# Kernel tuning notes

Hardware: AMD Instinct MI355X
Metric: run time of the kernel (lower is better)

Reference implementation:

```python
import jax, jax.numpy as jnp
import numpy as np

B, N, E = 8, 100000, 3200000
LAMBDA_PHYSICS = 1.0

def setup_inputs() -> dict:
    key = jax.random.key(0)
    k1, k2, k3, k4, k5 = jax.random.split(key, 5)
    node_heads = jax.random.normal(k1, (B, N), dtype=jnp.float32)
    demands = jax.random.normal(k2, (B, N), dtype=jnp.float32)
    edge_index = jax.random.randint(k3, (2, E), 0, N, dtype=jnp.int64)
    edge_attr = jax.random.uniform(k4, (E, 2), dtype=jnp.float32)
    reservoir_nodes = jax.random.randint(k5, (64,), 0, N, dtype=jnp.int64)
    reservoir_head = jnp.ones((1,), dtype=jnp.float32)
    return {"node_heads": node_heads, "demands": demands, "edge_index": edge_index,
            "edge_attr": edge_attr, "reservoir_nodes": reservoir_nodes,
            "reservoir_head": reservoir_head}

def reference(node_heads, demands, edge_index, edge_attr, reservoir_nodes, reservoir_head):
    src, dst = edge_index[0], edge_index[1]
    conductances = edge_attr[:, 0]  # [E]
    # Pipe flow: Q_e = g_e * (h_src - h_dst), shape [B, E]
    head_diff = node_heads[:, src] - node_heads[:, dst]
    flows = conductances[None, :] * head_diff
    # Continuity: vectorized scatter-add replacing the per-edge Python loop
    net_flows = jnp.zeros_like(node_heads).at[:, src].add(flows).at[:, dst].add(-flows)
    violations = net_flows - demands
    continuity_loss = jnp.mean(violations ** 2)
    # Boundary: reservoir heads pinned to reservoir_head
    pred_res = node_heads[:, reservoir_nodes]  # [B, n_res]
    boundary_loss = jnp.mean((pred_res - reservoir_head[0]) ** 2)
    total_physics_loss = (continuity_loss + boundary_loss) * LAMBDA_PHYSICS
    return continuity_loss, boundary_loss, total_physics_loss, flows
```

## Files before the change

kernel.cpp:

```cpp
#include <hip/hip_runtime.h>

#define B 8
#define N 100000
#define NE 3200000
#define CHUNK2_LOG 7
#define CHUNK2 128
#define NCHUNK2 782
#define CAP2 9216
#define CAPH 4800
#define EPB 2048
#define RPB (2 * EPB)
#define SCANW 1024

typedef float f32x4 __attribute__((ext_vector_type(4)));
typedef unsigned u32x2 __attribute__((ext_vector_type(2)));

__device__ u32x2 g_rec2[(size_t)NCHUNK2 * CAP2];
__device__ int   g_cursor2[NCHUNK2];
__device__ float g_heads_t[N * B];
__device__ float g_accum;

__global__ __launch_bounds__(256) void zero_kernel() {
    for (int i = threadIdx.x; i < NCHUNK2; i += 256) g_cursor2[i] = 0;
    if (threadIdx.x == 0) g_accum = 0.0f;
}

__global__ __launch_bounds__(256) void transpose_kernel(
    const float* __restrict__ node_heads)
{
    int i = blockIdx.x * blockDim.x + threadIdx.x;
    if (i >= N * B) return;
    int n = i >> 3, b = i & 7;
    g_heads_t[i] = node_heads[b * N + n];
}

__global__ __launch_bounds__(256) void phase1_kernel(
    const int* __restrict__ edge_index,
    const float* __restrict__ edge_attr,
    float* __restrict__ flows_out)
{
    __shared__ int   hist[NCHUNK2];
    __shared__ int   lbase[NCHUNK2];
    __shared__ int   gbase[NCHUNK2];
    __shared__ int   lcur[NCHUNK2];
    __shared__ int   scanbuf[SCANW];
    __shared__ u32x2 s_rec[RPB];

    int tid = threadIdx.x;
    int e0 = blockIdx.x * EPB;

    for (int i = tid; i < NCHUNK2; i += 256) hist[i] = 0;
    __syncthreads();

    for (int i = tid; i < EPB; i += 256) {
        int e = e0 + i;
        if (e < NE) {
            int s = edge_index[e];
            int d = edge_index[NE + e];
            atomicAdd(&hist[s >> CHUNK2_LOG], 1);
            atomicAdd(&hist[d >> CHUNK2_LOG], 1);
        }
    }
    __syncthreads();

    for (int i = tid; i < SCANW; i += 256)
        scanbuf[i] = (i < NCHUNK2) ? hist[i] : 0;
    __syncthreads();
    for (int off = 1; off < SCANW; off <<= 1) {
        int v[SCANW / 256];
#pragma unroll
        for (int j = 0; j < SCANW / 256; ++j) {
            int i = tid + j * 256;
            v[j] = (i >= off) ? scanbuf[i - off] : 0;
        }
        __syncthreads();
#pragma unroll
        for (int j = 0; j < SCANW / 256; ++j) {
            int i = tid + j * 256;
            if (i >= off) scanbuf[i] += v[j];
        }
        __syncthreads();
    }
    for (int i = tid; i < NCHUNK2; i += 256) {
        int lb = scanbuf[i] - hist[i];
        lbase[i] = lb;
        lcur[i]  = lb;
        gbase[i] = atomicAdd(&g_cursor2[i], hist[i]);
    }
    __syncthreads();

    for (int i = tid; i < EPB; i += 256) {
        int e = e0 + i;
        if (e >= NE) continue;
        int s = edge_index[e];
        int d = edge_index[NE + e];
        float c = edge_attr[2 * (size_t)e];

        const f32x4* hs4 = (const f32x4*)&g_heads_t[s << 3];
        const f32x4* hd4 = (const f32x4*)&g_heads_t[d << 3];
        f32x4 a0 = hs4[0], a1 = hs4[1];
        f32x4 b0 = hd4[0], b1 = hd4[1];
        f32x4 f0 = c * (a0 - b0);
        f32x4 f1 = c * (a1 - b1);

        __builtin_nontemporal_store(f0.x, &flows_out[0 * NE + e]);
        __builtin_nontemporal_store(f0.y, &flows_out[1 * NE + e]);
        __builtin_nontemporal_store(f0.z, &flows_out[2 * NE + e]);
        __builtin_nontemporal_store(f0.w, &flows_out[3 * NE + e]);
        __builtin_nontemporal_store(f1.x, &flows_out[4 * NE + e]);
        __builtin_nontemporal_store(f1.y, &flows_out[5 * NE + e]);
        __builtin_nontemporal_store(f1.z, &flows_out[6 * NE + e]);
        __builtin_nontemporal_store(f1.w, &flows_out[7 * NE + e]);

        unsigned cb = __float_as_uint(c);
        int ks = s >> CHUNK2_LOG;
        int sl = atomicAdd(&lcur[ks], 1);
        u32x2 rs; rs.x = ((unsigned)(s & (CHUNK2 - 1)) << 17) | (unsigned)d; rs.y = cb;
        s_rec[sl] = rs;
        int kd = d >> CHUNK2_LOG;
        sl = atomicAdd(&lcur[kd], 1);
        u32x2 rd; rd.x = ((unsigned)(d & (CHUNK2 - 1)) << 17) | (unsigned)s; rd.y = cb;
        s_rec[sl] = rd;
    }
    __syncthreads();

    int wave = tid >> 6, lane = tid & 63;
    for (int k = wave; k < NCHUNK2; k += 4) {
        int cnt = hist[k];
        if (cnt == 0) continue;
        int lb = lbase[k], gb = gbase[k];
        u32x2* dst = &g_rec2[(size_t)k * CAP2];
        for (int i = lane; i < cnt; i += 64) {
            if (gb + i < CAP2)
                __builtin_nontemporal_store(s_rec[lb + i], &dst[gb + i]);
        }
    }
}

__global__ __launch_bounds__(256) void sortgather_kernel(
    const float* __restrict__ demands)
{
    __shared__ u32x2 s_rec[CAPH];
    __shared__ int   hist[64];
    __shared__ int   hbase[64];
    __shared__ int   hcur[64];
    __shared__ int   scanbuf[64];
    __shared__ float wred[4];

    int tid = threadIdx.x;
    int c = blockIdx.x;
    int cnt = g_cursor2[c];
    if (cnt > CAP2) cnt = CAP2;
    const u32x2* rec = &g_rec2[(size_t)c * CAP2];

    float contrib = 0.0f;

    for (int h = 0; h < 2; ++h) {
        if (tid < 64) hist[tid] = 0;
        __syncthreads();

        for (int i = tid; i < cnt; i += 256) {
            int ml = (int)(rec[i].x >> 17);
            if ((ml >> 6) == h) atomicAdd(&hist[ml & 63], 1);
        }
        __syncthreads();

        if (tid < 64) scanbuf[tid] = hist[tid];
        __syncthreads();
        for (int off = 1; off < 64; off <<= 1) {
            int v = (tid < 64 && tid >= off) ? scanbuf[tid - off] : 0;
            __syncthreads();
            if (tid < 64 && tid >= off) scanbuf[tid] += v;
            __syncthreads();
        }
        if (tid < 64) {
            int b0 = scanbuf[tid] - hist[tid];
            hbase[tid] = b0;
            hcur[tid]  = b0;
        }
        __syncthreads();

        for (int i = tid; i < cnt; i += 256) {
            u32x2 r = rec[i];
            int ml = (int)(r.x >> 17);
            if ((ml >> 6) == h) {
                int sl = atomicAdd(&hcur[ml & 63], 1);
                if (sl < CAPH) {
                    u32x2 rr; rr.x = r.x & 0x1FFFFu; rr.y = r.y;
                    s_rec[sl] = rr;
                }
            }
        }
        __syncthreads();

        int nl = tid >> 2, p = tid & 3;
        int n = (c << CHUNK2_LOG) + (h << 6) + nl;
        int off0 = hbase[nl];
        int cn = hist[nl];
        if (off0 + cn > CAPH) cn = (CAPH > off0) ? (CAPH - off0) : 0;
        int nc = (n < N) ? n : 0;
        const f32x4* hm = (const f32x4*)&g_heads_t[nc << 3];
        f32x4 m0 = hm[0], m1 = hm[1];
        f32x4 a0 = {0.f, 0.f, 0.f, 0.f};
        f32x4 a1 = {0.f, 0.f, 0.f, 0.f};
        for (int i = p; i < cn; i += 4) {
            u32x2 r = s_rec[off0 + i];
            float cc = __uint_as_float(r.y);
            const f32x4* ho = (const f32x4*)&g_heads_t[r.x << 3];
            f32x4 o0 = ho[0], o1 = ho[1];
            a0 += cc * (m0 - o0);
            a1 += cc * (m1 - o1);
        }
        float acc[8] = {a0.x, a0.y, a0.z, a0.w, a1.x, a1.y, a1.z, a1.w};
        bool emit = (p == 0) && (n < N);
#pragma unroll
        for (int j = 0; j < 8; ++j) {
            float v = acc[j];
            v += __shfl_xor(v, 1, 64);
            v += __shfl_xor(v, 2, 64);
            if (emit) {
                float vv = v - demands[j * N + n];
                contrib = fmaf(vv, vv, contrib);
            }
        }
        __syncthreads();
    }

    for (int off = 32; off > 0; off >>= 1)
        contrib += __shfl_down(contrib, off, 64);
    int wave = tid >> 6, lane = tid & 63;
    if (lane == 0) wred[wave] = contrib;
    __syncthreads();
    if (tid == 0)
        unsafeAtomicAdd(&g_accum, wred[0] + wred[1] + wred[2] + wred[3]);
}

__global__ __launch_bounds__(512) void finalize_kernel(
    const float* __restrict__ node_heads,
    const int* __restrict__ res_nodes,
    const float* __restrict__ res_head,
    float* __restrict__ out)
{
    __shared__ float ssum[8];
    int t = threadIdx.x;
    int b = t >> 6;
    int j = t & 63;
    float pred = node_heads[b * N + res_nodes[j]];
    float diff = pred - res_head[0];
    float local = diff * diff;
    for (int off = 32; off > 0; off >>= 1)
        local += __shfl_down(local, off, 64);
    if ((t & 63) == 0) ssum[t >> 6] = local;
    __syncthreads();
    if (t == 0) {
        float bsum = 0.0f;
        for (int w = 0; w < 8; ++w) bsum += ssum[w];
        float boundary = bsum / 512.0f;
        float continuity = g_accum / (float)(B * N);
        out[0] = continuity;
        out[1] = boundary;
        out[2] = continuity + boundary;
    }
}

extern "C" void kernel_launch(void* const* d_in, const int* in_sizes, int n_in,
                              void* d_out, int out_size, void* d_ws, size_t ws_size,
                              hipStream_t stream) {
    const float* node_heads = (const float*)d_in[0];
    const float* demands    = (const float*)d_in[1];
    const int*   edge_index = (const int*)d_in[2];
    const float* edge_attr  = (const float*)d_in[3];
    const int*   res_nodes  = (const int*)d_in[4];
    const float* res_head   = (const float*)d_in[5];

    float* out = (float*)d_out;

    zero_kernel<<<1, 256, 0, stream>>>();
    transpose_kernel<<<(N * B + 255) / 256, 256, 0, stream>>>(node_heads);
    phase1_kernel<<<(NE + EPB - 1) / EPB, 256, 0, stream>>>(
        edge_index, edge_attr, out + 3);
    sortgather_kernel<<<NCHUNK2, 256, 0, stream>>>(demands);
    finalize_kernel<<<1, 512, 0, stream>>>(node_heads, res_nodes, res_head, out);
}
```

Baseline: 501.7 us.

## Replace shared-memory atomics with wave-ballot match aggregation in both bucketing kernels

```diff
diff --git a/kernel.cpp b/kernel.cpp
--- a/kernel.cpp
+++ b/kernel.cpp
@@ -7,9 +7,9 @@
 #define CHUNK2 128
 #define NCHUNK2 782
 #define CAP2 9216
-#define CAPH 4800
 #define EPB 2048
 #define RPB (2 * EPB)
+#define NWIN (EPB / 64)
 #define SCANW 1024
 
 typedef float f32x4 __attribute__((ext_vector_type(4)));
@@ -39,32 +39,56 @@
     const float* __restrict__ edge_attr,
     float* __restrict__ flows_out)
 {
-    __shared__ int   hist[NCHUNK2];
-    __shared__ int   lbase[NCHUNK2];
+    __shared__ u32x2 s_rec[RPB];
+    __shared__ int   wh[4 * NCHUNK2];
+    __shared__ int   lbase[NCHUNK2 + 1];
     __shared__ int   gbase[NCHUNK2];
-    __shared__ int   lcur[NCHUNK2];
-    __shared__ int   scanbuf[SCANW];
-    __shared__ u32x2 s_rec[RPB];
-
-    int tid = threadIdx.x;
+
+    int tid  = threadIdx.x;
+    int wave = tid >> 6, lane = tid & 63;
+    unsigned long long lanebit = 1ull << lane;
     int e0 = blockIdx.x * EPB;
 
-    for (int i = tid; i < NCHUNK2; i += 256) hist[i] = 0;
-    __syncthreads();
-
-    for (int i = tid; i < EPB; i += 256) {
-        int e = e0 + i;
-        if (e < NE) {
-            int s = edge_index[e];
-            int d = edge_index[NE + e];
-            atomicAdd(&hist[s >> CHUNK2_LOG], 1);
-            atomicAdd(&hist[d >> CHUNK2_LOG], 1);
-        }
-    }
-    __syncthreads();
-
-    for (int i = tid; i < SCANW; i += 256)
-        scanbuf[i] = (i < NCHUNK2) ? hist[i] : 0;
+    for (int i = tid; i < 4 * NCHUNK2; i += 256) wh[i] = 0;
+    __syncthreads();
+
+    for (int t = wave; t < NWIN; t += 4) {
+        int idx = t * 64 + lane;
+        int e = e0 + idx;
+        bool v = e < NE;
+        int s = 0, d = 0;
+        if (v) { s = edge_index[e]; d = edge_index[NE + e]; }
+        unsigned long long vm = __ballot(v);
+
+        unsigned ks = (unsigned)s >> CHUNK2_LOG;
+        unsigned long long m = vm;
+#pragma unroll
+        for (int b = 0; b < 10; ++b) {
+            unsigned long long bal = __ballot((ks >> b) & 1);
+            m &= ((ks >> b) & 1) ? bal : ~bal;
+        }
+        int ldr = m ? (__ffsll(m) - 1) : 0;
+        if (v && lane == ldr) wh[wave * NCHUNK2 + ks] += __popcll(m);
+
+        unsigned kd = (unsigned)d >> CHUNK2_LOG;
+        unsigned long long m2 = vm;
+#pragma unroll
+        for (int b = 0; b < 10; ++b) {
+            unsigned long long bal = __ballot((kd >> b) & 1);
+            m2 &= ((kd >> b) & 1) ? bal : ~bal;
+        }
+        int ldr2 = m2 ? (__ffsll(m2) - 1) : 0;
+        if (v && lane == ldr2) wh[wave * NCHUNK2 + kd] += __popcll(m2);
+    }
+    __syncthreads();
+
+    int* scanbuf = (int*)s_rec;
+    for (int i = tid; i < SCANW; i += 256) {
+        int tot = 0;
+        if (i < NCHUNK2)
+            tot = wh[i] + wh[NCHUNK2 + i] + wh[2 * NCHUNK2 + i] + wh[3 * NCHUNK2 + i];
+        scanbuf[i] = tot;
+    }
     __syncthreads();
     for (int off = 1; off < SCANW; off <<= 1) {
         int v[SCANW / 256];
@@ -81,54 +105,97 @@
         }
         __syncthreads();
     }
-    for (int i = tid; i < NCHUNK2; i += 256) {
-        int lb = scanbuf[i] - hist[i];
-        lbase[i] = lb;
-        lcur[i]  = lb;
-        gbase[i] = atomicAdd(&g_cursor2[i], hist[i]);
-    }
-    __syncthreads();
-
-    for (int i = tid; i < EPB; i += 256) {
-        int e = e0 + i;
-        if (e >= NE) continue;
-        int s = edge_index[e];
-        int d = edge_index[NE + e];
-        float c = edge_attr[2 * (size_t)e];
-
-        const f32x4* hs4 = (const f32x4*)&g_heads_t[s << 3];
-        const f32x4* hd4 = (const f32x4*)&g_heads_t[d << 3];
-        f32x4 a0 = hs4[0], a1 = hs4[1];
-        f32x4 b0 = hd4[0], b1 = hd4[1];
-        f32x4 f0 = c * (a0 - b0);
-        f32x4 f1 = c * (a1 - b1);
-
-        __builtin_nontemporal_store(f0.x, &flows_out[0 * NE + e]);
-        __builtin_nontemporal_store(f0.y, &flows_out[1 * NE + e]);
-        __builtin_nontemporal_store(f0.z, &flows_out[2 * NE + e]);
-        __builtin_nontemporal_store(f0.w, &flows_out[3 * NE + e]);
-        __builtin_nontemporal_store(f1.x, &flows_out[4 * NE + e]);
-        __builtin_nontemporal_store(f1.y, &flows_out[5 * NE + e]);
-        __builtin_nontemporal_store(f1.z, &flows_out[6 * NE + e]);
-        __builtin_nontemporal_store(f1.w, &flows_out[7 * NE + e]);
-
-        unsigned cb = __float_as_uint(c);
-        int ks = s >> CHUNK2_LOG;
-        int sl = atomicAdd(&lcur[ks], 1);
-        u32x2 rs; rs.x = ((unsigned)(s & (CHUNK2 - 1)) << 17) | (unsigned)d; rs.y = cb;
-        s_rec[sl] = rs;
-        int kd = d >> CHUNK2_LOG;
-        sl = atomicAdd(&lcur[kd], 1);
-        u32x2 rd; rd.x = ((unsigned)(d & (CHUNK2 - 1)) << 17) | (unsigned)s; rd.y = cb;
-        s_rec[sl] = rd;
-    }
-    __syncthreads();
-
-    int wave = tid >> 6, lane = tid & 63;
+    for (int k = tid; k < NCHUNK2; k += 256) {
+        int c0 = wh[k], c1 = wh[NCHUNK2 + k], c2 = wh[2 * NCHUNK2 + k], c3 = wh[3 * NCHUNK2 + k];
+        int tot = c0 + c1 + c2 + c3;
+        int incl = scanbuf[k];
+        int lb = incl - tot;
+        lbase[k] = lb;
+        if (k == NCHUNK2 - 1) lbase[NCHUNK2] = incl;
+        wh[k] = lb;
+        wh[NCHUNK2 + k] = lb + c0;
+        wh[2 * NCHUNK2 + k] = lb + c0 + c1;
+        wh[3 * NCHUNK2 + k] = lb + c0 + c1 + c2;
+        gbase[k] = atomicAdd(&g_cursor2[k], tot);
+    }
+    __syncthreads();
+
+    for (int t = wave; t < NWIN; t += 4) {
+        int idx = t * 64 + lane;
+        int e = e0 + idx;
+        bool v = e < NE;
+        int s = 0, d = 0; float cond = 0.0f;
+        if (v) {
+            s = edge_index[e];
+            d = edge_index[NE + e];
+            cond = edge_attr[2 * (size_t)e];
+        }
+        if (v) {
+            const f32x4* hs4 = (const f32x4*)&g_heads_t[s << 3];
+            const f32x4* hd4 = (const f32x4*)&g_heads_t[d << 3];
+            f32x4 a0 = hs4[0], a1 = hs4[1];
+            f32x4 b0 = hd4[0], b1 = hd4[1];
+            f32x4 f0 = cond * (a0 - b0);
+            f32x4 f1 = cond * (a1 - b1);
+            __builtin_nontemporal_store(f0.x, &flows_out[0 * NE + e]);
+            __builtin_nontemporal_store(f0.y, &flows_out[1 * NE + e]);
+            __builtin_nontemporal_store(f0.z, &flows_out[2 * NE + e]);
+            __builtin_nontemporal_store(f0.w, &flows_out[3 * NE + e]);
+            __builtin_nontemporal_store(f1.x, &flows_out[4 * NE + e]);
+            __builtin_nontemporal_store(f1.y, &flows_out[5 * NE + e]);
+            __builtin_nontemporal_store(f1.z, &flows_out[6 * NE + e]);
+            __builtin_nontemporal_store(f1.w, &flows_out[7 * NE + e]);
+        }
+        unsigned cb = __float_as_uint(cond);
+        unsigned long long vm = __ballot(v);
+
+        unsigned ks = (unsigned)s >> CHUNK2_LOG;
+        unsigned long long m = vm;
+#pragma unroll
+        for (int b = 0; b < 10; ++b) {
+            unsigned long long bal = __ballot((ks >> b) & 1);
+            m &= ((ks >> b) & 1) ? bal : ~bal;
+        }
+        int ldr = m ? (__ffsll(m) - 1) : 0;
+        int old = 0;
+        if (v && lane == ldr) {
+            int* p = &wh[wave * NCHUNK2 + ks];
+            old = *p; *p = old + __popcll(m);
+        }
+        old = __shfl(old, ldr, 64);
+        if (v) {
+            int slot = old + __popcll(m & (lanebit - 1));
+            u32x2 rr; rr.x = ((unsigned)(s & (CHUNK2 - 1)) << 17) | (unsigned)d; rr.y = cb;
+            s_rec[slot] = rr;
+        }
+
+        unsigned kd = (unsigned)d >> CHUNK2_LOG;
+        unsigned long long m2 = vm;
+#pragma unroll
+        for (int b = 0; b < 10; ++b) {
+            unsigned long long bal = __ballot((kd >> b) & 1);
+            m2 &= ((kd >> b) & 1) ? bal : ~bal;
+        }
+        int ldr2 = m2 ? (__ffsll(m2) - 1) : 0;
+        int old2 = 0;
+        if (v && lane == ldr2) {
+            int* p = &wh[wave * NCHUNK2 + kd];
+            old2 = *p; *p = old2 + __popcll(m2);
+        }
+        old2 = __shfl(old2, ldr2, 64);
+        if (v) {
+            int slot = old2 + __popcll(m2 & (lanebit - 1));
+            u32x2 rr; rr.x = ((unsigned)(d & (CHUNK2 - 1)) << 17) | (unsigned)s; rr.y = cb;
+            s_rec[slot] = rr;
+        }
+    }
+    __syncthreads();
+
     for (int k = wave; k < NCHUNK2; k += 4) {
-        int cnt = hist[k];
+        int lb = lbase[k];
+        int cnt = lbase[k + 1] - lb;
         if (cnt == 0) continue;
-        int lb = lbase[k], gb = gbase[k];
+        int gb = gbase[k];
         u32x2* dst = &g_rec2[(size_t)k * CAP2];
         for (int i = lane; i < cnt; i += 64) {
             if (gb + i < CAP2)
@@ -140,76 +207,124 @@
 __global__ __launch_bounds__(256) void sortgather_kernel(
     const float* __restrict__ demands)
 {
-    __shared__ u32x2 s_rec[CAPH];
-    __shared__ int   hist[64];
-    __shared__ int   hbase[64];
-    __shared__ int   hcur[64];
-    __shared__ int   scanbuf[64];
+    __shared__ u32x2 s_rec[CAP2];
+    __shared__ int   wh[4 * CHUNK2];
+    __shared__ int   hist[CHUNK2];
+    __shared__ int   hbase[CHUNK2];
+    __shared__ int   scanbuf[CHUNK2];
     __shared__ float wred[4];
 
-    int tid = threadIdx.x;
+    int tid  = threadIdx.x;
+    int wave = tid >> 6, lane = tid & 63;
+    unsigned long long lanebit = 1ull << lane;
     int c = blockIdx.x;
     int cnt = g_cursor2[c];
     if (cnt > CAP2) cnt = CAP2;
     const u32x2* rec = &g_rec2[(size_t)c * CAP2];
+    int nwin = (cnt + 63) >> 6;
+
+    for (int i = tid; i < 4 * CHUNK2; i += 256) wh[i] = 0;
+    __syncthreads();
+
+    for (int t = wave; t < nwin; t += 4) {
+        int i = t * 64 + lane;
+        bool v = i < cnt;
+        unsigned key = 0;
+        if (v) key = rec[i].x >> 17;
+        unsigned long long m = __ballot(v);
+#pragma unroll
+        for (int b = 0; b < 7; ++b) {
+            unsigned long long bal = __ballot((key >> b) & 1);
+            m &= ((key >> b) & 1) ? bal : ~bal;
+        }
+        int ldr = m ? (__ffsll(m) - 1) : 0;
+        if (v && lane == ldr) wh[wave * CHUNK2 + key] += __popcll(m);
+    }
+    __syncthreads();
+
+    if (tid < CHUNK2) {
+        int c0 = wh[tid], c1 = wh[CHUNK2 + tid], c2 = wh[2 * CHUNK2 + tid], c3 = wh[3 * CHUNK2 + tid];
+        int tot = c0 + c1 + c2 + c3;
+        hist[tid] = tot;
+        scanbuf[tid] = tot;
+    }
+    __syncthreads();
+    for (int off = 1; off < CHUNK2; off <<= 1) {
+        int vv = (tid < CHUNK2 && tid >= off) ? scanbuf[tid - off] : 0;
+        __syncthreads();
+        if (tid < CHUNK2 && tid >= off) scanbuf[tid] += vv;
+        __syncthreads();
+    }
+    if (tid < CHUNK2) {
+        int lb = scanbuf[tid] - hist[tid];
+        hbase[tid] = lb;
+        int c0 = wh[tid], c1 = wh[CHUNK2 + tid], c2 = wh[2 * CHUNK2 + tid];
+        wh[tid] = lb;
+        wh[CHUNK2 + tid] = lb + c0;
+        wh[2 * CHUNK2 + tid] = lb + c0 + c1;
+        wh[3 * CHUNK2 + tid] = lb + c0 + c1 + c2;
+    }
+    __syncthreads();
+
+    for (int t = wave; t < nwin; t += 4) {
+        int i = t * 64 + lane;
+        bool v = i < cnt;
+        u32x2 r; r.x = 0; r.y = 0;
+        if (v) r = rec[i];
+        unsigned key = r.x >> 17;
+        unsigned long long m = __ballot(v);
+#pragma unroll
+        for (int b = 0; b < 7; ++b) {
+            unsigned long long bal = __ballot((key >> b) & 1);
+            m &= ((key >> b) & 1) ? bal : ~bal;
+        }
+        int ldr = m ? (__ffsll(m) - 1) : 0;
+        int old = 0;
+        if (v && lane == ldr) {
+            int* p = &wh[wave * CHUNK2 + key];
+            old = *p; *p = old + __popcll(m);
+        }
+        old = __shfl(old, ldr, 64);
+        if (v) {
+            int slot = old + __popcll(m & (lanebit - 1));
+            s_rec[slot] = r;
+        }
+    }
+    __syncthreads();
 
     float contrib = 0.0f;
-
-    for (int h = 0; h < 2; ++h) {
-        if (tid < 64) hist[tid] = 0;
-        __syncthreads();
-
-        for (int i = tid; i < cnt; i += 256) {
-            int ml = (int)(rec[i].x >> 17);
-            if ((ml >> 6) == h) atomicAdd(&hist[ml & 63], 1);
-        }
-        __syncthreads();
-
-        if (tid < 64) scanbuf[tid] = hist[tid];
-        __syncthreads();
-        for (int off = 1; off < 64; off <<= 1) {
-            int v = (tid < 64 && tid >= off) ? scanbuf[tid - off] : 0;
-            __syncthreads();
-            if (tid < 64 && tid >= off) scanbuf[tid] += v;
-            __syncthreads();
-        }
-        if (tid < 64) {
-            int b0 = scanbuf[tid] - hist[tid];
-            hbase[tid] = b0;
-            hcur[tid]  = b0;
-        }
-        __syncthreads();
-
-        for (int i = tid; i < cnt; i += 256) {
-            u32x2 r = rec[i];
-            int ml = (int)(r.x >> 17);
-            if ((ml >> 6) == h) {
-                int sl = atomicAdd(&hcur[ml & 63], 1);
-                if (sl < CAPH) {
-                    u32x2 rr; rr.x = r.x & 0x1FFFFu; rr.y = r.y;
-                    s_rec[sl] = rr;
-                }
-            }
-        }
-        __syncthreads();
-
-        int nl = tid >> 2, p = tid & 3;
-        int n = (c << CHUNK2_LOG) + (h << 6) + nl;
+    {
+        int nl = tid >> 1, p = tid & 1;
+        int n = (c << CHUNK2_LOG) + nl;
         int off0 = hbase[nl];
         int cn = hist[nl];
-        if (off0 + cn > CAPH) cn = (CAPH > off0) ? (CAPH - off0) : 0;
         int nc = (n < N) ? n : 0;
         const f32x4* hm = (const f32x4*)&g_heads_t[nc << 3];
         f32x4 m0 = hm[0], m1 = hm[1];
         f32x4 a0 = {0.f, 0.f, 0.f, 0.f};
         f32x4 a1 = {0.f, 0.f, 0.f, 0.f};
-        for (int i = p; i < cn; i += 4) {
-            u32x2 r = s_rec[off0 + i];
-            float cc = __uint_as_float(r.y);
-            const f32x4* ho = (const f32x4*)&g_heads_t[r.x << 3];
-            f32x4 o0 = ho[0], o1 = ho[1];
-            a0 += cc * (m0 - o0);
-            a1 += cc * (m1 - o1);
+        int i = p;
+        for (; i + 2 < cn; i += 4) {
+            u32x2 r0 = s_rec[off0 + i];
+            u32x2 r1 = s_rec[off0 + i + 2];
+            float c0 = __uint_as_float(r0.y);
+            float c1 = __uint_as_float(r1.y);
+            const f32x4* ho0 = (const f32x4*)&g_heads_t[(r0.x & 0x1FFFFu) << 3];
+            const f32x4* ho1 = (const f32x4*)&g_heads_t[(r1.x & 0x1FFFFu) << 3];
+            f32x4 o00 = ho0[0], o01 = ho0[1];
+            f32x4 o10 = ho1[0], o11 = ho1[1];
+            a0 += c0 * (m0 - o00);
+            a1 += c0 * (m1 - o01);
+            a0 += c1 * (m0 - o10);
+            a1 += c1 * (m1 - o11);
+        }
+        for (; i < cn; i += 2) {
+            u32x2 r0 = s_rec[off0 + i];
+            float c0 = __uint_as_float(r0.y);
+            const f32x4* ho0 = (const f32x4*)&g_heads_t[(r0.x & 0x1FFFFu) << 3];
+            f32x4 o00 = ho0[0], o01 = ho0[1];
+            a0 += c0 * (m0 - o00);
+            a1 += c0 * (m1 - o01);
         }
         float acc[8] = {a0.x, a0.y, a0.z, a0.w, a1.x, a1.y, a1.z, a1.w};
         bool emit = (p == 0) && (n < N);
@@ -217,18 +332,15 @@
         for (int j = 0; j < 8; ++j) {
             float v = acc[j];
             v += __shfl_xor(v, 1, 64);
-            v += __shfl_xor(v, 2, 64);
             if (emit) {
                 float vv = v - demands[j * N + n];
                 contrib = fmaf(vv, vv, contrib);
             }
         }
-        __syncthreads();
     }
 
     for (int off = 32; off > 0; off >>= 1)
         contrib += __shfl_down(contrib, off, 64);
-    int wave = tid >> 6, lane = tid & 63;
     if (lane == 0) wred[wave] = contrib;
     __syncthreads();
     if (tid == 0)
```

Result: slower. 542.2 us (+8.1%).

## Sort whole chunk in one LDS pass instead of two half passes

Applied to the files above, without the earlier changes.

```diff
diff --git a/kernel.cpp b/kernel.cpp
--- a/kernel.cpp
+++ b/kernel.cpp
@@ -7,7 +7,6 @@
 #define CHUNK2 128
 #define NCHUNK2 782
 #define CAP2 9216
-#define CAPH 4800
 #define EPB 2048
 #define RPB (2 * EPB)
 #define SCANW 1024
@@ -132,7 +131,7 @@
         u32x2* dst = &g_rec2[(size_t)k * CAP2];
         for (int i = lane; i < cnt; i += 64) {
             if (gb + i < CAP2)
-                __builtin_nontemporal_store(s_rec[lb + i], &dst[gb + i]);
+                dst[gb + i] = s_rec[lb + i];
         }
     }
 }
@@ -140,76 +139,82 @@
 __global__ __launch_bounds__(256) void sortgather_kernel(
     const float* __restrict__ demands)
 {
-    __shared__ u32x2 s_rec[CAPH];
-    __shared__ int   hist[64];
-    __shared__ int   hbase[64];
-    __shared__ int   hcur[64];
-    __shared__ int   scanbuf[64];
+    __shared__ u32x2 s_rec[CAP2];
+    __shared__ int   hist[CHUNK2];
+    __shared__ int   hbase[CHUNK2];
+    __shared__ int   hcur[CHUNK2];
+    __shared__ int   scanbuf[CHUNK2];
     __shared__ float wred[4];
 
-    int tid = threadIdx.x;
+    int tid  = threadIdx.x;
+    int wave = tid >> 6, lane = tid & 63;
     int c = blockIdx.x;
     int cnt = g_cursor2[c];
     if (cnt > CAP2) cnt = CAP2;
     const u32x2* rec = &g_rec2[(size_t)c * CAP2];
 
+    if (tid < CHUNK2) hist[tid] = 0;
+    __syncthreads();
+
+    for (int i = tid; i < cnt; i += 256)
+        atomicAdd(&hist[rec[i].x >> 17], 1);
+    __syncthreads();
+
+    if (tid < CHUNK2) scanbuf[tid] = hist[tid];
+    __syncthreads();
+    for (int off = 1; off < CHUNK2; off <<= 1) {
+        int v = (tid < CHUNK2 && tid >= off) ? scanbuf[tid - off] : 0;
+        __syncthreads();
+        if (tid < CHUNK2 && tid >= off) scanbuf[tid] += v;
+        __syncthreads();
+    }
+    if (tid < CHUNK2) {
+        int lb = scanbuf[tid] - hist[tid];
+        hbase[tid] = lb;
+        hcur[tid]  = lb;
+    }
+    __syncthreads();
+
+    for (int i = tid; i < cnt; i += 256) {
+        u32x2 r = rec[i];
+        int sl = atomicAdd(&hcur[r.x >> 17], 1);
+        s_rec[sl] = r;
+    }
+    __syncthreads();
+
     float contrib = 0.0f;
-
-    for (int h = 0; h < 2; ++h) {
-        if (tid < 64) hist[tid] = 0;
-        __syncthreads();
-
-        for (int i = tid; i < cnt; i += 256) {
-            int ml = (int)(rec[i].x >> 17);
-            if ((ml >> 6) == h) atomicAdd(&hist[ml & 63], 1);
-        }
-        __syncthreads();
-
-        if (tid < 64) scanbuf[tid] = hist[tid];
-        __syncthreads();
-        for (int off = 1; off < 64; off <<= 1) {
-            int v = (tid < 64 && tid >= off) ? scanbuf[tid - off] : 0;
-            __syncthreads();
-            if (tid < 64 && tid >= off) scanbuf[tid] += v;
-            __syncthreads();
-        }
-        if (tid < 64) {
-            int b0 = scanbuf[tid] - hist[tid];
-            hbase[tid] = b0;
-            hcur[tid]  = b0;
-        }
-        __syncthreads();
-
-        for (int i = tid; i < cnt; i += 256) {
-            u32x2 r = rec[i];
-            int ml = (int)(r.x >> 17);
-            if ((ml >> 6) == h) {
-                int sl = atomicAdd(&hcur[ml & 63], 1);
-                if (sl < CAPH) {
-                    u32x2 rr; rr.x = r.x & 0x1FFFFu; rr.y = r.y;
-                    s_rec[sl] = rr;
-                }
-            }
-        }
-        __syncthreads();
-
-        int nl = tid >> 2, p = tid & 3;
-        int n = (c << CHUNK2_LOG) + (h << 6) + nl;
+    {
+        int nl = tid >> 1, p = tid & 1;
+        int n = (c << CHUNK2_LOG) + nl;
         int off0 = hbase[nl];
         int cn = hist[nl];
-        if (off0 + cn > CAPH) cn = (CAPH > off0) ? (CAPH - off0) : 0;
         int nc = (n < N) ? n : 0;
         const f32x4* hm = (const f32x4*)&g_heads_t[nc << 3];
         f32x4 m0 = hm[0], m1 = hm[1];
         f32x4 a0 = {0.f, 0.f, 0.f, 0.f};
         f32x4 a1 = {0.f, 0.f, 0.f, 0.f};
-        for (int i = p; i < cn; i += 4) {
-            u32x2 r = s_rec[off0 + i];
-            float cc = __uint_as_float(r.y);
-            const f32x4* ho = (const f32x4*)&g_heads_t[r.x << 3];
-            f32x4 o0 = ho[0], o1 = ho[1];
-            a0 += cc * (m0 - o0);
-            a1 += cc * (m1 - o1);
+        int i = p;
+        for (; i + 2 < cn; i += 4) {
+            u32x2 r0 = s_rec[off0 + i];
+            u32x2 r1 = s_rec[off0 + i + 2];
+            float c0 = __uint_as_float(r0.y);
+            float c1 = __uint_as_float(r1.y);
+            const f32x4* ho0 = (const f32x4*)&g_heads_t[(r0.x & 0x1FFFFu) << 3];
+            const f32x4* ho1 = (const f32x4*)&g_heads_t[(r1.x & 0x1FFFFu) << 3];
+            f32x4 o00 = ho0[0], o01 = ho0[1];
+            f32x4 o10 = ho1[0], o11 = ho1[1];
+            a0 += c0 * (m0 - o00);
+            a1 += c0 * (m1 - o01);
+            a0 += c1 * (m0 - o10);
+            a1 += c1 * (m1 - o11);
+        }
+        for (; i < cn; i += 2) {
+            u32x2 r0 = s_rec[off0 + i];
+            float c0 = __uint_as_float(r0.y);
+            const f32x4* ho0 = (const f32x4*)&g_heads_t[(r0.x & 0x1FFFFu) << 3];
+            f32x4 o00 = ho0[0], o01 = ho0[1];
+            a0 += c0 * (m0 - o00);
+            a1 += c0 * (m1 - o01);
         }
         float acc[8] = {a0.x, a0.y, a0.z, a0.w, a1.x, a1.y, a1.z, a1.w};
         bool emit = (p == 0) && (n < N);
@@ -217,18 +222,15 @@
         for (int j = 0; j < 8; ++j) {
             float v = acc[j];
             v += __shfl_xor(v, 1, 64);
-            v += __shfl_xor(v, 2, 64);
             if (emit) {
                 float vv = v - demands[j * N + n];
                 contrib = fmaf(vv, vv, contrib);
             }
         }
-        __syncthreads();
     }
 
     for (int off = 32; off > 0; off >>= 1)
         contrib += __shfl_down(contrib, off, 64);
-    int wave = tid >> 6, lane = tid & 63;
     if (lane == 0) wred[wave] = contrib;
     __syncthreads();
     if (tid == 0)
```

Measured after the change: 480.3 us. 1.04x faster.
